# Performance work log

Measured on AMD Instinct MI355X. Metric: run time of the kernel, lower is better.

Reference implementation:

```python
import jax, jax.numpy as jnp
import numpy as np

B, N = 2048, 8192
K = 64          # subset size / number of relaxation steps
TAU = 1.0
EPS = 1e-10


def setup_inputs() -> dict:
    key = jax.random.key(0)
    k1, k2 = jax.random.split(key)
    scores = jax.random.normal(k1, (B, N), dtype=jnp.float32)
    # Gumbel(0,1) noise, same as torch.distributions.Gumbel(zeros, ones).sample()
    u = jax.random.uniform(k2, (B, N), dtype=jnp.float32, minval=1e-20, maxval=1.0)
    g = -jnp.log(-jnp.log(u))
    return {"scores": scores, "g": g}


def reference(scores, g):
    # Perturb scores with Gumbel noise
    s0 = scores + g  # [B, N]
    khot0 = jnp.zeros_like(s0)
    onehot0 = jnp.zeros_like(s0)

    def step(carry, _):
        s, khot, onehot_approx = carry
        khot_mask = jnp.maximum(1.0 - onehot_approx, EPS)   # suppress picked items
        s = s + jnp.log(khot_mask)
        onehot_approx = jax.nn.softmax(s / TAU, axis=1)
        return (s, khot + onehot_approx, onehot_approx), None

    (_, khot, _), _ = jax.lax.scan(step, (s0, khot0, onehot0), None, length=K)
    # hard=False -> return relaxed k-hot vector
    return khot
```

## Files before the change

### kernel.cpp

```cpp
#include <hip/hip_runtime.h>
#include <math.h>


#define BROWS 2048
#define NCOLS 8192
#define KSTEPS 64

#define THREADS 256
#define EPT (NCOLS / THREADS)
#define NWAVE (THREADS / 64)

__device__ __forceinline__ float wave_sum_dpp(float x) {
    int t;
    t = __builtin_amdgcn_update_dpp(0, __builtin_bit_cast(int, x), 0x111, 0xf, 0xf, true);
    x += __builtin_bit_cast(float, t);
    t = __builtin_amdgcn_update_dpp(0, __builtin_bit_cast(int, x), 0x112, 0xf, 0xf, true);
    x += __builtin_bit_cast(float, t);
    t = __builtin_amdgcn_update_dpp(0, __builtin_bit_cast(int, x), 0x114, 0xf, 0xf, true);
    x += __builtin_bit_cast(float, t);
    t = __builtin_amdgcn_update_dpp(0, __builtin_bit_cast(int, x), 0x118, 0xf, 0xf, true);
    x += __builtin_bit_cast(float, t);
    t = __builtin_amdgcn_update_dpp(0, __builtin_bit_cast(int, x), 0x142, 0xa, 0xf, false);
    x += __builtin_bit_cast(float, t);
    t = __builtin_amdgcn_update_dpp(0, __builtin_bit_cast(int, x), 0x143, 0xc, 0xf, false);
    x += __builtin_bit_cast(float, t);
    return __builtin_bit_cast(float, __builtin_amdgcn_readlane(__builtin_bit_cast(int, x), 63));
}

__global__ __launch_bounds__(THREADS, 2) void gumbel_subset_kernel(
    const float* __restrict__ scores,
    const float* __restrict__ g,
    float* __restrict__ out)
{
    const int row = blockIdx.x;
    const int t = threadIdx.x;
    const float* __restrict__ srow = scores + (size_t)row * NCOLS;
    const float* __restrict__ grow = g + (size_t)row * NCOLS;
    float* __restrict__ orow = out + (size_t)row * NCOLS;

    float v[EPT];
    float kh[EPT];

    float m = -INFINITY;
#pragma unroll
    for (int c = 0; c < EPT / 4; ++c) {
        const int idx = c * (THREADS * 4) + t * 4;
        const float4 a = *reinterpret_cast<const float4*>(srow + idx);
        const float4 b = *reinterpret_cast<const float4*>(grow + idx);
        const float s0 = a.x + b.x;
        const float s1 = a.y + b.y;
        const float s2 = a.z + b.z;
        const float s3 = a.w + b.w;
        v[c * 4 + 0] = s0;
        v[c * 4 + 1] = s1;
        v[c * 4 + 2] = s2;
        v[c * 4 + 3] = s3;
        m = fmaxf(m, fmaxf(fmaxf(s0, s1), fmaxf(s2, s3)));
    }

    __shared__ float red[2][NWAVE];
    const int wave = t >> 6;
    const int lane = t & 63;

#pragma unroll
    for (int off = 32; off > 0; off >>= 1)
        m = fmaxf(m, __shfl_xor(m, off, 64));
    if (lane == 0) red[0][wave] = m;
    __syncthreads();
    m = fmaxf(fmaxf(red[0][0], red[0][1]), fmaxf(red[0][2], red[0][3]));
    __syncthreads();

    float sa = 0.0f, sb = 0.0f, sc = 0.0f, sd = 0.0f;
#pragma unroll
    for (int e = 0; e < EPT; e += 4) {
        v[e + 0] = __expf(v[e + 0] - m);
        v[e + 1] = __expf(v[e + 1] - m);
        v[e + 2] = __expf(v[e + 2] - m);
        v[e + 3] = __expf(v[e + 3] - m);
        kh[e + 0] = 0.0f; kh[e + 1] = 0.0f; kh[e + 2] = 0.0f; kh[e + 3] = 0.0f;
        sa += v[e + 0]; sb += v[e + 1]; sc += v[e + 2]; sd += v[e + 3];
    }

#pragma unroll 2
    for (int it = 0; it < KSTEPS; ++it) {
        const float s = wave_sum_dpp((sa + sb) + (sc + sd));

        const int buf = it & 1;
        if (lane == 0) red[buf][wave] = s;
        __syncthreads();
        const float S = (red[buf][0] + red[buf][1]) + (red[buf][2] + red[buf][3]);
        const float rinv = __builtin_amdgcn_rcpf(S);

        sa = 0.0f; sb = 0.0f; sc = 0.0f; sd = 0.0f;
#pragma unroll
        for (int e = 0; e < EPT; e += 4) {
            const float w0 = v[e + 0] * rinv;
            const float w1 = v[e + 1] * rinv;
            const float w2 = v[e + 2] * rinv;
            const float w3 = v[e + 3] * rinv;
            kh[e + 0] += w0; kh[e + 1] += w1; kh[e + 2] += w2; kh[e + 3] += w3;
            v[e + 0] = __builtin_fmaf(-w0, v[e + 0], v[e + 0]);
            v[e + 1] = __builtin_fmaf(-w1, v[e + 1], v[e + 1]);
            v[e + 2] = __builtin_fmaf(-w2, v[e + 2], v[e + 2]);
            v[e + 3] = __builtin_fmaf(-w3, v[e + 3], v[e + 3]);
            sa += v[e + 0]; sb += v[e + 1]; sc += v[e + 2]; sd += v[e + 3];
        }
    }

#pragma unroll
    for (int c = 0; c < EPT / 4; ++c) {
        const int idx = c * (THREADS * 4) + t * 4;
        float4 o;
        o.x = kh[c * 4 + 0];
        o.y = kh[c * 4 + 1];
        o.z = kh[c * 4 + 2];
        o.w = kh[c * 4 + 3];
        *reinterpret_cast<float4*>(orow + idx) = o;
    }
}

extern "C" void kernel_launch(void* const* d_in, const int* in_sizes, int n_in,
                              void* d_out, int out_size, void* d_ws, size_t ws_size,
                              hipStream_t stream) {
    const float* scores = (const float*)d_in[0];
    const float* g = (const float*)d_in[1];
    float* out = (float*)d_out;
    (void)in_sizes; (void)n_in; (void)out_size; (void)d_ws; (void)ws_size;

    gumbel_subset_kernel<<<BROWS, THREADS, 0, stream>>>(scores, g, out);
}
```

Measured before the change: 101.1 us.

## Pack k-hot accumulators into fp16 pairs and re-read inputs to raise occupancy

Stores the per-element k-hot accumulator as packed half2 values, updated with cvt_pkrtz and pk_add_f16, which halves its register footprint. The max pass no longer keeps the perturbed scores in registers; the second pass reloads both inputs from global memory to compute the exponentials. Launch bounds go from 2 to 5 blocks per SIMD-level occupancy target so more rows can be resident at once. The cost is a second read of the inputs and reduced accumulator precision: fp16 sums of up to 64 small contributions may lose accuracy against the fp32 reference.

```diff
diff --git a/kernel.cpp b/kernel.cpp
--- a/kernel.cpp
+++ b/kernel.cpp
@@ -1,6 +1,8 @@
 #include <hip/hip_runtime.h>
 #include <math.h>
 
+
+typedef _Float16 h2 __attribute__((ext_vector_type(2)));
 
 #define BROWS 2048
 #define NCOLS 8192
@@ -8,6 +10,7 @@
 
 #define THREADS 256
 #define EPT (NCOLS / THREADS)
+#define NPAIR (EPT / 2)
 #define NWAVE (THREADS / 64)
 
 __device__ __forceinline__ float wave_sum_dpp(float x) {
@@ -27,7 +30,7 @@
     return __builtin_bit_cast(float, __builtin_amdgcn_readlane(__builtin_bit_cast(int, x), 63));
 }
 
-__global__ __launch_bounds__(THREADS, 2) void gumbel_subset_kernel(
+__global__ __launch_bounds__(THREADS, 5) void gumbel_subset_kernel(
     const float* __restrict__ scores,
     const float* __restrict__ g,
     float* __restrict__ out)
@@ -38,8 +41,9 @@
     const float* __restrict__ grow = g + (size_t)row * NCOLS;
     float* __restrict__ orow = out + (size_t)row * NCOLS;
 
-    float v[EPT];
-    float kh[EPT];
+    __shared__ float red[2][NWAVE];
+    const int wave = t >> 6;
+    const int lane = t & 63;
 
     float m = -INFINITY;
 #pragma unroll
@@ -47,20 +51,9 @@
         const int idx = c * (THREADS * 4) + t * 4;
         const float4 a = *reinterpret_cast<const float4*>(srow + idx);
         const float4 b = *reinterpret_cast<const float4*>(grow + idx);
-        const float s0 = a.x + b.x;
-        const float s1 = a.y + b.y;
-        const float s2 = a.z + b.z;
-        const float s3 = a.w + b.w;
-        v[c * 4 + 0] = s0;
-        v[c * 4 + 1] = s1;
-        v[c * 4 + 2] = s2;
-        v[c * 4 + 3] = s3;
-        m = fmaxf(m, fmaxf(fmaxf(s0, s1), fmaxf(s2, s3)));
+        m = fmaxf(m, fmaxf(fmaxf(a.x + b.x, a.y + b.y),
+                           fmaxf(a.z + b.z, a.w + b.w)));
     }
-
-    __shared__ float red[2][NWAVE];
-    const int wave = t >> 6;
-    const int lane = t & 63;
 
 #pragma unroll
     for (int off = 32; off > 0; off >>= 1)
@@ -70,15 +63,22 @@
     m = fmaxf(fmaxf(red[0][0], red[0][1]), fmaxf(red[0][2], red[0][3]));
     __syncthreads();
 
+    float v[EPT];
+    h2 kh[NPAIR];
     float sa = 0.0f, sb = 0.0f, sc = 0.0f, sd = 0.0f;
 #pragma unroll
-    for (int e = 0; e < EPT; e += 4) {
-        v[e + 0] = __expf(v[e + 0] - m);
-        v[e + 1] = __expf(v[e + 1] - m);
-        v[e + 2] = __expf(v[e + 2] - m);
-        v[e + 3] = __expf(v[e + 3] - m);
-        kh[e + 0] = 0.0f; kh[e + 1] = 0.0f; kh[e + 2] = 0.0f; kh[e + 3] = 0.0f;
-        sa += v[e + 0]; sb += v[e + 1]; sc += v[e + 2]; sd += v[e + 3];
+    for (int c = 0; c < EPT / 4; ++c) {
+        const int idx = c * (THREADS * 4) + t * 4;
+        const float4 a = *reinterpret_cast<const float4*>(srow + idx);
+        const float4 b = *reinterpret_cast<const float4*>(grow + idx);
+        v[c * 4 + 0] = __expf(a.x + b.x - m);
+        v[c * 4 + 1] = __expf(a.y + b.y - m);
+        v[c * 4 + 2] = __expf(a.z + b.z - m);
+        v[c * 4 + 3] = __expf(a.w + b.w - m);
+        kh[2 * c + 0] = (h2){(_Float16)0.0f, (_Float16)0.0f};
+        kh[2 * c + 1] = (h2){(_Float16)0.0f, (_Float16)0.0f};
+        sa += v[c * 4 + 0]; sb += v[c * 4 + 1];
+        sc += v[c * 4 + 2]; sd += v[c * 4 + 3];
     }
 
 #pragma unroll 2
@@ -93,17 +93,29 @@
 
         sa = 0.0f; sb = 0.0f; sc = 0.0f; sd = 0.0f;
 #pragma unroll
-        for (int e = 0; e < EPT; e += 4) {
-            const float w0 = v[e + 0] * rinv;
-            const float w1 = v[e + 1] * rinv;
-            const float w2 = v[e + 2] * rinv;
-            const float w3 = v[e + 3] * rinv;
-            kh[e + 0] += w0; kh[e + 1] += w1; kh[e + 2] += w2; kh[e + 3] += w3;
-            v[e + 0] = __builtin_fmaf(-w0, v[e + 0], v[e + 0]);
-            v[e + 1] = __builtin_fmaf(-w1, v[e + 1], v[e + 1]);
-            v[e + 2] = __builtin_fmaf(-w2, v[e + 2], v[e + 2]);
-            v[e + 3] = __builtin_fmaf(-w3, v[e + 3], v[e + 3]);
-            sa += v[e + 0]; sb += v[e + 1]; sc += v[e + 2]; sd += v[e + 3];
+        for (int q = 0; q < NPAIR; q += 2) {
+            {
+                const float w0 = v[2 * q + 0] * rinv;
+                const float w1 = v[2 * q + 1] * rinv;
+                h2 pkw, kn;
+                asm("v_cvt_pkrtz_f16_f32 %0, %1, %2" : "=&v"(pkw) : "v"(w0), "v"(w1));
+                asm("v_pk_add_f16 %0, %1, %2" : "=&v"(kn) : "v"(kh[q]), "v"(pkw));
+                kh[q] = kn;
+                v[2 * q + 0] = __builtin_fmaf(-w0, v[2 * q + 0], v[2 * q + 0]);
+                v[2 * q + 1] = __builtin_fmaf(-w1, v[2 * q + 1], v[2 * q + 1]);
+                sa += v[2 * q + 0]; sb += v[2 * q + 1];
+            }
+            {
+                const float w0 = v[2 * q + 2] * rinv;
+                const float w1 = v[2 * q + 3] * rinv;
+                h2 pkw, kn;
+                asm("v_cvt_pkrtz_f16_f32 %0, %1, %2" : "=&v"(pkw) : "v"(w0), "v"(w1));
+                asm("v_pk_add_f16 %0, %1, %2" : "=&v"(kn) : "v"(kh[q + 1]), "v"(pkw));
+                kh[q + 1] = kn;
+                v[2 * q + 2] = __builtin_fmaf(-w0, v[2 * q + 2], v[2 * q + 2]);
+                v[2 * q + 3] = __builtin_fmaf(-w1, v[2 * q + 3], v[2 * q + 3]);
+                sc += v[2 * q + 2]; sd += v[2 * q + 3];
+            }
         }
     }
 
@@ -111,10 +123,10 @@
     for (int c = 0; c < EPT / 4; ++c) {
         const int idx = c * (THREADS * 4) + t * 4;
         float4 o;
-        o.x = kh[c * 4 + 0];
-        o.y = kh[c * 4 + 1];
-        o.z = kh[c * 4 + 2];
-        o.w = kh[c * 4 + 3];
+        o.x = (float)kh[2 * c + 0].x;
+        o.y = (float)kh[2 * c + 0].y;
+        o.z = (float)kh[2 * c + 1].x;
+        o.w = (float)kh[2 * c + 1].y;
         *reinterpret_cast<float4*>(orow + idx) = o;
     }
 }
```

Result: slower. 116.8 us (+15.5%).
